# Performance work log

Measured on AMD Instinct MI355X. Metric: run time of the kernel, lower is better.

The kernel has to match this reference:

```python
import jax, jax.numpy as jnp
import numpy as np

DIM, H, DH, MLP, ADIM = 512, 8, 64, 2048, 256
B, T = 4, 2048
EPS = 1e-5


def setup_inputs() -> dict:
    key = jax.random.key(0)
    ks = jax.random.split(key, 10)
    s = 0.02
    inner = H * DH
    return {
        "x": jax.random.normal(ks[0], (B, T, DIM), jnp.float32),
        "action_emb": jax.random.normal(ks[1], (B, T, ADIM), jnp.float32),
        "causal_mask": jnp.tril(jnp.ones((T, T), dtype=bool)),
        "Wqkv": jax.random.normal(ks[2], (3 * inner, DIM), jnp.float32) * s,
        "Wout": jax.random.normal(ks[3], (DIM, inner), jnp.float32) * s,
        "bout": jnp.zeros((DIM,), jnp.float32),
        "W1": jax.random.normal(ks[4], (MLP, DIM), jnp.float32) * s,
        "b1": jnp.zeros((MLP,), jnp.float32),
        "W2": jax.random.normal(ks[5], (DIM, MLP), jnp.float32) * s,
        "b2": jnp.zeros((DIM,), jnp.float32),
        # adaLN is zero-init in the module; use small random so modulation is exercised
        "Wmod": jax.random.normal(ks[6], (6 * DIM, ADIM), jnp.float32) * s,
        "bmod": jnp.zeros((6 * DIM,), jnp.float32),
    }


def _layernorm(z):
    mu = jnp.mean(z, axis=-1, keepdims=True)
    var = jnp.var(z, axis=-1, keepdims=True)
    return (z - mu) * jax.lax.rsqrt(var + EPS)


def reference(x, action_emb, causal_mask, Wqkv, Wout, bout, W1, b1, W2, b2, Wmod, bmod):
    b, t, d = x.shape
    mod = jax.nn.silu(action_emb) @ Wmod.T + bmod            # (B,T,6*dim)
    shift1, scale1, gate1, shift2, scale2, gate2 = jnp.split(mod, 6, axis=-1)

    h = _layernorm(x) * (1.0 + scale1) + shift1
    qkv = (h @ Wqkv.T).reshape(b, t, 3, H, DH)
    q, k, v = qkv[:, :, 0], qkv[:, :, 1], qkv[:, :, 2]        # (B,T,H,DH)
    scores = jnp.einsum("bqhd,bkhd->bhqk", q, k) * (DH ** -0.5)
    scores = jnp.where(causal_mask, scores, -jnp.inf)
    attn = jax.nn.softmax(scores, axis=-1)                   # dropout=eval (identity)
    h = jnp.einsum("bhqk,bkhd->bqhd", attn, v).reshape(b, t, H * DH)
    h = h @ Wout.T + bout
    x = x + gate1 * h

    h = _layernorm(x) * (1.0 + scale2) + shift2
    h = jax.nn.gelu(h @ W1.T + b1, approximate=False) @ W2.T + b2
    return x + gate2 * h
```

## Files before the change

kernel.cpp:

```cpp
#include <hip/hip_runtime.h>
#include <math.h>
#include <stdint.h>

#define BB 4
#define TT 2048
#define NTOK 8192
#define DIMD 512
#define HH 8
#define DHH 64
#define MLPD 2048
#define ADIMD 256
#define MODD 3072
#define LNEPS 1e-5f
#define LOG2E_8 0.18033688011112042f

typedef short short8 __attribute__((ext_vector_type(8)));
typedef unsigned short ushort4v __attribute__((ext_vector_type(4)));
typedef __bf16 bf16x8 __attribute__((ext_vector_type(8)));
typedef float f32x4 __attribute__((ext_vector_type(4)));

static __device__ __forceinline__ unsigned short f2bf(float f) {
    union { float f; unsigned u; } v; v.f = f;
    unsigned r = v.u + 0x7fffu + ((v.u >> 16) & 1u);
    return (unsigned short)(r >> 16);
}
static __device__ __forceinline__ float bf2f(unsigned short u) {
    union { unsigned u; float f; } v; v.u = (unsigned)u << 16; return v.f;
}

static __device__ __forceinline__ f32x4 mfma_bf16(short8 a, short8 b, f32x4 c) {
    return __builtin_amdgcn_mfma_f32_16x16x32_bf16(
        __builtin_bit_cast(bf16x8, a), __builtin_bit_cast(bf16x8, b), c, 0, 0, 0);
}

struct CvtArgs {
    const float* s[6];
    unsigned short* d[6];
    int cum[7];
};
__global__ __launch_bounds__(256) void cvt_all(CvtArgs a)
{
    const int i = blockIdx.x * 256 + threadIdx.x;
    if (i >= a.cum[6]) return;
    int seg = 0;
    #pragma unroll
    for (int k = 1; k < 6; k++) seg += (i >= a.cum[k]);
    const int off = i - a.cum[seg];
    float4 v = ((const float4*)a.s[seg])[off];
    if (seg == 5) {
        v.x = v.x / (1.f + __expf(-v.x));
        v.y = v.y / (1.f + __expf(-v.y));
        v.z = v.z / (1.f + __expf(-v.z));
        v.w = v.w / (1.f + __expf(-v.w));
    }
    ushort4v o = { f2bf(v.x), f2bf(v.y), f2bf(v.z), f2bf(v.w) };
    ((ushort4v*)a.d[seg])[off] = o;
}

template<int EPI, int BN>
__global__ __launch_bounds__(256) void gemm_bf16(
    const unsigned short* __restrict__ A, const unsigned short* __restrict__ Bw,
    const float* __restrict__ bias, const float* __restrict__ res,
    const unsigned short* __restrict__ mod,
    int M, int N, int K,
    void* __restrict__ Cv)
{
    constexpr int MT = (BN == 128) ? 4 : 2;
    constexpr int NPB = (BN == 128) ? 4 : 2;
    __shared__ unsigned short As[128 * 72];
    __shared__ unsigned short Bs[BN * 72];

    const int tid = threadIdx.x;
    const int w = tid >> 6, lane = tid & 63;
    const int quad = lane >> 4, l16 = lane & 15;
    const int wrow = (BN == 128) ? (w >> 1) * 64 : w * 32;
    const int wcol = (BN == 128) ? (w & 1) * 64 : 0;
    const int row0 = blockIdx.y * 128, col0 = blockIdx.x * BN;

    const int srow = tid >> 3;
    const int skc  = (tid & 7) * 8;

    f32x4 acc[MT][4];
    #pragma unroll
    for (int i = 0; i < MT; i++)
        #pragma unroll
        for (int j = 0; j < 4; j++) acc[i][j] = (f32x4){0.f, 0.f, 0.f, 0.f};

    short8 pA[4], pB[NPB];
    auto prefetch = [&](int k0) {
        #pragma unroll
        for (int p = 0; p < 4; p++)
            pA[p] = *(const short8*)&A[(size_t)(row0 + srow + p * 32) * K + k0 + skc];
        #pragma unroll
        for (int p = 0; p < NPB; p++)
            pB[p] = *(const short8*)&Bw[(size_t)(col0 + srow + p * 32) * K + k0 + skc];
    };
    auto stage = [&]() {
        #pragma unroll
        for (int p = 0; p < 4; p++)
            *(short8*)&As[(srow + p * 32) * 72 + skc] = pA[p];
        #pragma unroll
        for (int p = 0; p < NPB; p++)
            *(short8*)&Bs[(srow + p * 32) * 72 + skc] = pB[p];
    };

    prefetch(0);
    stage();
    __syncthreads();

    for (int k0 = 0; k0 < K; k0 += 64) {
        const bool more = (k0 + 64 < K);
        if (more) prefetch(k0 + 64);

        #pragma unroll
        for (int ks = 0; ks < 2; ks++) {
            short8 af[MT], bf[4];
            #pragma unroll
            for (int mt = 0; mt < MT; mt++)
                af[mt] = *(const short8*)&As[(wrow + mt * 16 + l16) * 72 + ks * 32 + quad * 8];
            #pragma unroll
            for (int nt = 0; nt < 4; nt++)
                bf[nt] = *(const short8*)&Bs[(wcol + nt * 16 + l16) * 72 + ks * 32 + quad * 8];
            #pragma unroll
            for (int nt = 0; nt < 4; nt++)
                #pragma unroll
                for (int mt = 0; mt < MT; mt++)
                    acc[mt][nt] = mfma_bf16(af[mt], bf[nt], acc[mt][nt]);
        }
        __syncthreads();
        if (more) stage();
        __syncthreads();
    }

    float* Cf = (float*)Cv;
    unsigned short* Cb = (unsigned short*)Cv;
    #pragma unroll
    for (int mt = 0; mt < MT; mt++) {
        #pragma unroll
        for (int r = 0; r < 4; r++) {
            const int row = row0 + wrow + mt * 16 + quad * 4 + r;
            #pragma unroll
            for (int nt = 0; nt < 4; nt++) {
                const int col = col0 + wcol + nt * 16 + l16;
                const size_t idx = (size_t)row * N + col;
                const float v = acc[mt][nt][r];
                if (EPI == 0) {
                    Cb[idx] = f2bf(v);
                } else if (EPI == 2) {
                    float t = v + bias[col];
                    Cb[idx] = f2bf(0.5f * t * (1.f + erff(t * 0.70710678118654752f)));
                } else if (EPI == 3) {
                    float t = v + bias[col];
                    Cf[idx] = res[idx] + bf2f(mod[(size_t)row * MODD + 1024 + col]) * t;
                } else if (EPI == 4) {
                    float t = v + bias[col];
                    Cf[idx] = Cf[idx] + bf2f(mod[(size_t)row * MODD + 2560 + col]) * t;
                } else if (EPI == 5) {
                    Cb[idx] = f2bf(v + bias[col]);
                }
            }
        }
    }
}

__global__ __launch_bounds__(256) void adaln_ln(
    const float* __restrict__ src, const unsigned short* __restrict__ mod,
    unsigned short* __restrict__ dst, int shift_off, int scale_off)
{
    const int n = blockIdx.x;
    const int tid = threadIdx.x;
    const float* xr = src + (size_t)n * DIMD;
    float v0 = xr[tid], v1 = xr[tid + 256];
    float s = v0 + v1;
    float q = v0 * v0 + v1 * v1;
    #pragma unroll
    for (int o = 32; o > 0; o >>= 1) {
        s += __shfl_down(s, o);
        q += __shfl_down(q, o);
    }
    __shared__ float sh[8];
    __shared__ float mu_sh, rs_sh;
    const int wid = tid >> 6, lane = tid & 63;
    if (lane == 0) { sh[wid] = s; sh[wid + 4] = q; }
    __syncthreads();
    if (tid == 0) {
        float S = sh[0] + sh[1] + sh[2] + sh[3];
        float Q = sh[4] + sh[5] + sh[6] + sh[7];
        float mu = S * (1.f / DIMD);
        float var = Q * (1.f / DIMD) - mu * mu;
        mu_sh = mu;
        rs_sh = rsqrtf(var + LNEPS);
    }
    __syncthreads();
    const float mu = mu_sh, rs = rs_sh;
    const unsigned short* mrow = mod + (size_t)n * MODD;
    const size_t o0 = (size_t)n * DIMD + tid;
    dst[o0]       = f2bf((v0 - mu) * rs * (1.f + bf2f(mrow[scale_off + tid]))       + bf2f(mrow[shift_off + tid]));
    dst[o0 + 256] = f2bf((v1 - mu) * rs * (1.f + bf2f(mrow[scale_off + tid + 256])) + bf2f(mrow[shift_off + tid + 256]));
}

__global__ __launch_bounds__(256, 4) void attn_mfma(
    const unsigned short* __restrict__ qkv, unsigned short* __restrict__ outb)
{
    __shared__ unsigned short Kt[64][72];
    __shared__ unsigned short Vt[64][72];
    __shared__ unsigned short Ps[4][16][72];

    const int qi = (TT / 64 - 1) - blockIdx.x;
    const int h = blockIdx.y, b = blockIdx.z;
    const int tid = threadIdx.x;
    const int w = tid >> 6;
    const int lane = tid & 63;
    const int quad = lane >> 4;
    const int l16 = lane & 15;

    const int qw = qi * 64 + w * 16;
    const size_t tokbase = (size_t)b * TT;

    short8 qf[2];
    {
        const unsigned short* qp = qkv + (tokbase + qw + l16) * 1536 + h * 64 + quad * 8;
        #pragma unroll
        for (int hd = 0; hd < 2; hd++) {
            short8 raw = *(const short8*)(qp + hd * 32);
            short8 f;
            #pragma unroll
            for (int j = 0; j < 8; j++)
                f[j] = (short)f2bf(bf2f((unsigned short)raw[j]) * LOG2E_8);
            qf[hd] = f;
        }
    }

    f32x4 Oa[4];
    float mrun = -INFINITY, lrun = 0.f;
    #pragma unroll
    for (int mt = 0; mt < 4; mt++) Oa[mt] = (f32x4){0.f, 0.f, 0.f, 0.f};

    const int nkt = qi + 1;
    const int vk0 = (tid & 31) * 2;
    const int vdb = (tid >> 5) * 8;

    short8 kpre[2], vpre[2];
    auto prefetchKV = [&](int kt) {
        const unsigned short* kb = qkv + (tokbase + (size_t)kt * 64) * 1536 + 512 + h * 64;
        #pragma unroll
        for (int it = 0; it < 2; it++) {
            const int i = tid + it * 256;
            kpre[it] = *(const short8*)(kb + (size_t)(i >> 3) * 1536 + (i & 7) * 8);
        }
        const unsigned short* vb = qkv + (tokbase + (size_t)kt * 64 + vk0) * 1536 + 1024 + h * 64 + vdb;
        vpre[0] = *(const short8*)vb;
        vpre[1] = *(const short8*)(vb + 1536);
    };
    auto storeKV = [&]() {
        #pragma unroll
        for (int it = 0; it < 2; it++) {
            const int i = tid + it * 256;
            *(short8*)&Kt[i >> 3][(i & 7) * 8] = kpre[it];
        }
        #pragma unroll
        for (int j = 0; j < 8; j++) {
            *(unsigned*)&Vt[vdb + j][vk0] =
                (unsigned)(unsigned short)vpre[0][j]
                | ((unsigned)(unsigned short)vpre[1][j] << 16);
        }
    };

    prefetchKV(0);
    storeKV();
    __syncthreads();

    for (int kt = 0; kt < nkt; kt++) {
        const bool haveNext = (kt + 1 < nkt);
        if (haveNext) prefetchKV(kt + 1);

        f32x4 st[4];
        #pragma unroll
        for (int mk = 0; mk < 4; mk++) {
            const short8 a0 = *(const short8*)&Kt[mk * 16 + l16][quad * 8];
            const short8 a1 = *(const short8*)&Kt[mk * 16 + l16][32 + quad * 8];
            st[mk] = (f32x4){0.f, 0.f, 0.f, 0.f};
            st[mk] = mfma_bf16(a0, qf[0], st[mk]);
            st[mk] = mfma_bf16(a1, qf[1], st[mk]);
        }
        if (kt == qi) {
            const int qpos = qw + l16;
            #pragma unroll
            for (int mk = 0; mk < 4; mk++)
                #pragma unroll
                for (int r = 0; r < 4; r++)
                    if (kt * 64 + mk * 16 + quad * 4 + r > qpos) st[mk][r] = -INFINITY;
        }
        float tm = -INFINITY;
        #pragma unroll
        for (int mk = 0; mk < 4; mk++)
            #pragma unroll
            for (int r = 0; r < 4; r++) tm = fmaxf(tm, st[mk][r]);
        tm = fmaxf(tm, __shfl_xor(tm, 16));
        tm = fmaxf(tm, __shfl_xor(tm, 32));
        const float mn = fmaxf(mrun, tm);
        const float alpha = __builtin_amdgcn_exp2f(mrun - mn);
        mrun = mn;
        float ts = 0.f;
        #pragma unroll
        for (int mk = 0; mk < 4; mk++) {
            const float p0 = __builtin_amdgcn_exp2f(st[mk][0] - mn);
            const float p1 = __builtin_amdgcn_exp2f(st[mk][1] - mn);
            const float p2 = __builtin_amdgcn_exp2f(st[mk][2] - mn);
            const float p3 = __builtin_amdgcn_exp2f(st[mk][3] - mn);
            ts += (p0 + p1) + (p2 + p3);
            const unsigned long long pk =
                (unsigned long long)f2bf(p0)
                | ((unsigned long long)f2bf(p1) << 16)
                | ((unsigned long long)f2bf(p2) << 32)
                | ((unsigned long long)f2bf(p3) << 48);
            *(unsigned long long*)&Ps[w][l16][mk * 16 + quad * 4] = pk;
        }
        ts += __shfl_xor(ts, 16);
        ts += __shfl_xor(ts, 32);
        lrun = lrun * alpha + ts;
        #pragma unroll
        for (int mt = 0; mt < 4; mt++) Oa[mt] *= alpha;
        __threadfence_block();

        short8 pf[2];
        #pragma unroll
        for (int kc = 0; kc < 2; kc++)
            pf[kc] = *(const short8*)&Ps[w][l16][kc * 32 + quad * 8];
        #pragma unroll
        for (int mt = 0; mt < 4; mt++)
            #pragma unroll
            for (int kc = 0; kc < 2; kc++) {
                const short8 vf = *(const short8*)&Vt[mt * 16 + l16][kc * 32 + quad * 8];
                Oa[mt] = mfma_bf16(vf, pf[kc], Oa[mt]);
            }

        __syncthreads();
        if (haveNext) storeKV();
        __syncthreads();
    }

    {
        const float inv = 1.f / lrun;
        const size_t tok = tokbase + qw + l16;
        #pragma unroll
        for (int mt = 0; mt < 4; mt++) {
            const unsigned long long pk =
                (unsigned long long)f2bf(Oa[mt][0] * inv)
                | ((unsigned long long)f2bf(Oa[mt][1] * inv) << 16)
                | ((unsigned long long)f2bf(Oa[mt][2] * inv) << 32)
                | ((unsigned long long)f2bf(Oa[mt][3] * inv) << 48);
            *(unsigned long long*)&outb[tok * DIMD + h * 64 + mt * 16 + quad * 4] = pk;
        }
    }
}

extern "C" void kernel_launch(void* const* d_in, const int* in_sizes, int n_in,
                              void* d_out, int out_size, void* d_ws, size_t ws_size,
                              hipStream_t stream)
{
    (void)in_sizes; (void)n_in; (void)out_size; (void)ws_size;

    const float* x    = (const float*)d_in[0];
    const float* aemb = (const float*)d_in[1];
    const float* Wqkv = (const float*)d_in[3];
    const float* Wout = (const float*)d_in[4];
    const float* bout = (const float*)d_in[5];
    const float* W1   = (const float*)d_in[6];
    const float* b1   = (const float*)d_in[7];
    const float* W2   = (const float*)d_in[8];
    const float* b2   = (const float*)d_in[9];
    const float* Wmod = (const float*)d_in[10];
    const float* bmod = (const float*)d_in[11];

    float* out = (float*)d_out;

    char* p = (char*)d_ws;
    unsigned short* modw = (unsigned short*)p; p += (size_t)NTOK * MODD * 2;
    unsigned short* h12  = (unsigned short*)p; p += (size_t)NTOK * DIMD * 2;
    unsigned short* qkvb = (unsigned short*)p; p += (size_t)NTOK * 1536 * 2;
    unsigned short* attw = (unsigned short*)p; p += (size_t)NTOK * DIMD * 2;
    unsigned short* hid  = qkvb;
    unsigned short* sact = (unsigned short*)p; p += (size_t)NTOK * ADIMD * 2;
    unsigned short* wq = (unsigned short*)p;   p += (size_t)1536 * 512 * 2;
    unsigned short* wo = (unsigned short*)p;   p += (size_t)512 * 512 * 2;
    unsigned short* w1 = (unsigned short*)p;   p += (size_t)2048 * 512 * 2;
    unsigned short* w2 = (unsigned short*)p;   p += (size_t)512 * 2048 * 2;
    unsigned short* wm = (unsigned short*)p;   p += (size_t)3072 * 256 * 2;

    CvtArgs ca;
    ca.s[0] = Wqkv; ca.d[0] = wq;
    ca.s[1] = Wout; ca.d[1] = wo;
    ca.s[2] = W1;   ca.d[2] = w1;
    ca.s[3] = W2;   ca.d[3] = w2;
    ca.s[4] = Wmod; ca.d[4] = wm;
    ca.s[5] = aemb; ca.d[5] = sact;
    const int n4s[6] = {1536 * 512 / 4, 512 * 512 / 4, 2048 * 512 / 4,
                        512 * 2048 / 4, 3072 * 256 / 4, NTOK * ADIMD / 4};
    ca.cum[0] = 0;
    for (int i = 0; i < 6; i++) ca.cum[i + 1] = ca.cum[i] + n4s[i];
    cvt_all<<<(ca.cum[6] + 255) / 256, 256, 0, stream>>>(ca);

    gemm_bf16<5, 128><<<dim3(MODD / 128, NTOK / 128), 256, 0, stream>>>(
        sact, wm, bmod, nullptr, nullptr, NTOK, MODD, ADIMD, modw);

    adaln_ln<<<NTOK, 256, 0, stream>>>(x, modw, h12, 0, 512);

    gemm_bf16<0, 128><<<dim3(1536 / 128, NTOK / 128), 256, 0, stream>>>(
        h12, wq, nullptr, nullptr, nullptr, NTOK, 1536, DIMD, qkvb);

    attn_mfma<<<dim3(TT / 64, HH, BB), 256, 0, stream>>>(qkvb, attw);

    gemm_bf16<3, 64><<<dim3(DIMD / 64, NTOK / 128), 256, 0, stream>>>(
        attw, wo, bout, x, modw, NTOK, DIMD, DIMD, out);

    adaln_ln<<<NTOK, 256, 0, stream>>>(out, modw, h12, 1536, 2048);

    gemm_bf16<2, 128><<<dim3(MLPD / 128, NTOK / 128), 256, 0, stream>>>(
        h12, w1, b1, nullptr, nullptr, NTOK, MLPD, DIMD, hid);

    gemm_bf16<4, 64><<<dim3(DIMD / 64, NTOK / 128), 256, 0, stream>>>(
        hid, w2, b2, nullptr, modw, NTOK, DIMD, MLPD, out);
}
```

Before: 337.8 us.

## Deepen register prefetch to two tiles in GEMM and attention loops

Both the GEMM main loop and the flash-attention KV loop now keep two register-staged tiles in flight, so global loads run two iterations ahead instead of one. __syncthreads is replaced with a barrier that only waits on LDS counters, which lets outstanding global loads stay in flight across barriers. The goal is to hide more global-memory latency. The cost is roughly double the prefetch registers, which may lower occupancy, and the GEMM loop assumes an even K-tile count.

```diff
diff --git a/kernel.cpp b/kernel.cpp
--- a/kernel.cpp
+++ b/kernel.cpp
@@ -31,6 +31,10 @@
 static __device__ __forceinline__ f32x4 mfma_bf16(short8 a, short8 b, f32x4 c) {
     return __builtin_amdgcn_mfma_f32_16x16x32_bf16(
         __builtin_bit_cast(bf16x8, a), __builtin_bit_cast(bf16x8, b), c, 0, 0, 0);
+}
+
+static __device__ __forceinline__ void bar_lds() {
+    asm volatile("s_waitcnt lgkmcnt(0)\n\ts_barrier" ::: "memory");
 }
 
 struct CvtArgs {
@@ -86,51 +90,58 @@
         #pragma unroll
         for (int j = 0; j < 4; j++) acc[i][j] = (f32x4){0.f, 0.f, 0.f, 0.f};
 
-    short8 pA[4], pB[NPB];
-    auto prefetch = [&](int k0) {
-        #pragma unroll
-        for (int p = 0; p < 4; p++)
-            pA[p] = *(const short8*)&A[(size_t)(row0 + srow + p * 32) * K + k0 + skc];
-        #pragma unroll
-        for (int p = 0; p < NPB; p++)
-            pB[p] = *(const short8*)&Bw[(size_t)(col0 + srow + p * 32) * K + k0 + skc];
-    };
-    auto stage = [&]() {
-        #pragma unroll
-        for (int p = 0; p < 4; p++)
-            *(short8*)&As[(srow + p * 32) * 72 + skc] = pA[p];
-        #pragma unroll
-        for (int p = 0; p < NPB; p++)
-            *(short8*)&Bs[(srow + p * 32) * 72 + skc] = pB[p];
-    };
-
-    prefetch(0);
-    stage();
-    __syncthreads();
-
-    for (int k0 = 0; k0 < K; k0 += 64) {
-        const bool more = (k0 + 64 < K);
-        if (more) prefetch(k0 + 64);
-
-        #pragma unroll
-        for (int ks = 0; ks < 2; ks++) {
-            short8 af[MT], bf[4];
-            #pragma unroll
-            for (int mt = 0; mt < MT; mt++)
-                af[mt] = *(const short8*)&As[(wrow + mt * 16 + l16) * 72 + ks * 32 + quad * 8];
-            #pragma unroll
-            for (int nt = 0; nt < 4; nt++)
-                bf[nt] = *(const short8*)&Bs[(wcol + nt * 16 + l16) * 72 + ks * 32 + quad * 8];
-            #pragma unroll
-            for (int nt = 0; nt < 4; nt++)
-                #pragma unroll
-                for (int mt = 0; mt < MT; mt++)
-                    acc[mt][nt] = mfma_bf16(af[mt], bf[nt], acc[mt][nt]);
+    short8 a0[4], b0[NPB], a1[4], b1[NPB];
+
+#define G_LOAD(AS_, BS_, k0_) do {                                              \
+    _Pragma("unroll") for (int p = 0; p < 4; p++)                               \
+        AS_[p] = *(const short8*)&A[(size_t)(row0 + srow + p * 32) * K + (k0_) + skc]; \
+    _Pragma("unroll") for (int p = 0; p < NPB; p++)                             \
+        BS_[p] = *(const short8*)&Bw[(size_t)(col0 + srow + p * 32) * K + (k0_) + skc]; \
+} while (0)
+
+#define G_STAGE(AS_, BS_) do {                                                  \
+    _Pragma("unroll") for (int p = 0; p < 4; p++)                               \
+        *(short8*)&As[(srow + p * 32) * 72 + skc] = AS_[p];                     \
+    _Pragma("unroll") for (int p = 0; p < NPB; p++)                             \
+        *(short8*)&Bs[(srow + p * 32) * 72 + skc] = BS_[p];                     \
+} while (0)
+
+#define G_COMPUTE() do {                                                        \
+    _Pragma("unroll") for (int ks = 0; ks < 2; ks++) {                          \
+        short8 af[MT], bf[4];                                                   \
+        _Pragma("unroll") for (int mt = 0; mt < MT; mt++)                       \
+            af[mt] = *(const short8*)&As[(wrow + mt * 16 + l16) * 72 + ks * 32 + quad * 8]; \
+        _Pragma("unroll") for (int nt = 0; nt < 4; nt++)                        \
+            bf[nt] = *(const short8*)&Bs[(wcol + nt * 16 + l16) * 72 + ks * 32 + quad * 8]; \
+        _Pragma("unroll") for (int nt = 0; nt < 4; nt++)                        \
+            _Pragma("unroll") for (int mt = 0; mt < MT; mt++)                   \
+                acc[mt][nt] = mfma_bf16(af[mt], bf[nt], acc[mt][nt]);           \
+    }                                                                           \
+} while (0)
+
+    const int NK = K >> 6;
+    G_LOAD(a0, b0, 0);
+    G_LOAD(a1, b1, 64);
+    G_STAGE(a0, b0);
+    bar_lds();
+
+    for (int t = 0; t < NK; t += 2) {
+        if (t + 2 < NK) G_LOAD(a0, b0, (t + 2) << 6);
+        G_COMPUTE();
+        bar_lds();
+        G_STAGE(a1, b1);
+        bar_lds();
+        if (t + 3 < NK) G_LOAD(a1, b1, (t + 3) << 6);
+        G_COMPUTE();
+        if (t + 2 < NK) {
+            bar_lds();
+            G_STAGE(a0, b0);
+            bar_lds();
         }
-        __syncthreads();
-        if (more) stage();
-        __syncthreads();
-    }
+    }
+#undef G_LOAD
+#undef G_STAGE
+#undef G_COMPUTE
 
     float* Cf = (float*)Cv;
     unsigned short* Cb = (unsigned short*)Cv;
@@ -240,105 +251,105 @@
     const int vk0 = (tid & 31) * 2;
     const int vdb = (tid >> 5) * 8;
 
-    short8 kpre[2], vpre[2];
-    auto prefetchKV = [&](int kt) {
-        const unsigned short* kb = qkv + (tokbase + (size_t)kt * 64) * 1536 + 512 + h * 64;
-        #pragma unroll
-        for (int it = 0; it < 2; it++) {
-            const int i = tid + it * 256;
-            kpre[it] = *(const short8*)(kb + (size_t)(i >> 3) * 1536 + (i & 7) * 8);
-        }
-        const unsigned short* vb = qkv + (tokbase + (size_t)kt * 64 + vk0) * 1536 + 1024 + h * 64 + vdb;
-        vpre[0] = *(const short8*)vb;
-        vpre[1] = *(const short8*)(vb + 1536);
-    };
-    auto storeKV = [&]() {
-        #pragma unroll
-        for (int it = 0; it < 2; it++) {
-            const int i = tid + it * 256;
-            *(short8*)&Kt[i >> 3][(i & 7) * 8] = kpre[it];
-        }
-        #pragma unroll
-        for (int j = 0; j < 8; j++) {
-            *(unsigned*)&Vt[vdb + j][vk0] =
-                (unsigned)(unsigned short)vpre[0][j]
-                | ((unsigned)(unsigned short)vpre[1][j] << 16);
-        }
-    };
-
-    prefetchKV(0);
-    storeKV();
-    __syncthreads();
-
-    for (int kt = 0; kt < nkt; kt++) {
-        const bool haveNext = (kt + 1 < nkt);
-        if (haveNext) prefetchKV(kt + 1);
-
-        f32x4 st[4];
-        #pragma unroll
-        for (int mk = 0; mk < 4; mk++) {
-            const short8 a0 = *(const short8*)&Kt[mk * 16 + l16][quad * 8];
-            const short8 a1 = *(const short8*)&Kt[mk * 16 + l16][32 + quad * 8];
-            st[mk] = (f32x4){0.f, 0.f, 0.f, 0.f};
-            st[mk] = mfma_bf16(a0, qf[0], st[mk]);
-            st[mk] = mfma_bf16(a1, qf[1], st[mk]);
-        }
-        if (kt == qi) {
-            const int qpos = qw + l16;
-            #pragma unroll
-            for (int mk = 0; mk < 4; mk++)
-                #pragma unroll
-                for (int r = 0; r < 4; r++)
-                    if (kt * 64 + mk * 16 + quad * 4 + r > qpos) st[mk][r] = -INFINITY;
-        }
-        float tm = -INFINITY;
-        #pragma unroll
-        for (int mk = 0; mk < 4; mk++)
-            #pragma unroll
-            for (int r = 0; r < 4; r++) tm = fmaxf(tm, st[mk][r]);
-        tm = fmaxf(tm, __shfl_xor(tm, 16));
-        tm = fmaxf(tm, __shfl_xor(tm, 32));
-        const float mn = fmaxf(mrun, tm);
-        const float alpha = __builtin_amdgcn_exp2f(mrun - mn);
-        mrun = mn;
-        float ts = 0.f;
-        #pragma unroll
-        for (int mk = 0; mk < 4; mk++) {
-            const float p0 = __builtin_amdgcn_exp2f(st[mk][0] - mn);
-            const float p1 = __builtin_amdgcn_exp2f(st[mk][1] - mn);
-            const float p2 = __builtin_amdgcn_exp2f(st[mk][2] - mn);
-            const float p3 = __builtin_amdgcn_exp2f(st[mk][3] - mn);
-            ts += (p0 + p1) + (p2 + p3);
-            const unsigned long long pk =
-                (unsigned long long)f2bf(p0)
-                | ((unsigned long long)f2bf(p1) << 16)
-                | ((unsigned long long)f2bf(p2) << 32)
-                | ((unsigned long long)f2bf(p3) << 48);
-            *(unsigned long long*)&Ps[w][l16][mk * 16 + quad * 4] = pk;
-        }
-        ts += __shfl_xor(ts, 16);
-        ts += __shfl_xor(ts, 32);
-        lrun = lrun * alpha + ts;
-        #pragma unroll
-        for (int mt = 0; mt < 4; mt++) Oa[mt] *= alpha;
-        __threadfence_block();
-
-        short8 pf[2];
-        #pragma unroll
-        for (int kc = 0; kc < 2; kc++)
-            pf[kc] = *(const short8*)&Ps[w][l16][kc * 32 + quad * 8];
-        #pragma unroll
-        for (int mt = 0; mt < 4; mt++)
-            #pragma unroll
-            for (int kc = 0; kc < 2; kc++) {
-                const short8 vf = *(const short8*)&Vt[mt * 16 + l16][kc * 32 + quad * 8];
-                Oa[mt] = mfma_bf16(vf, pf[kc], Oa[mt]);
-            }
-
-        __syncthreads();
-        if (haveNext) storeKV();
-        __syncthreads();
-    }
+    short8 kp0[2], vp0[2], kp1[2], vp1[2];
+
+#define A_LOAD(KS_, VS_, kt_) do {                                              \
+    const unsigned short* kb = qkv + (tokbase + (size_t)(kt_) * 64) * 1536 + 512 + h * 64; \
+    _Pragma("unroll") for (int it = 0; it < 2; it++) {                          \
+        const int i = tid + it * 256;                                           \
+        KS_[it] = *(const short8*)(kb + (size_t)(i >> 3) * 1536 + (i & 7) * 8); \
+    }                                                                           \
+    const unsigned short* vb = qkv + (tokbase + (size_t)(kt_) * 64 + vk0) * 1536 + 1024 + h * 64 + vdb; \
+    VS_[0] = *(const short8*)vb;                                                \
+    VS_[1] = *(const short8*)(vb + 1536);                                       \
+} while (0)
+
+#define A_STAGE(KS_, VS_) do {                                                  \
+    _Pragma("unroll") for (int it = 0; it < 2; it++) {                          \
+        const int i = tid + it * 256;                                           \
+        *(short8*)&Kt[i >> 3][(i & 7) * 8] = KS_[it];                           \
+    }                                                                           \
+    _Pragma("unroll") for (int j = 0; j < 8; j++) {                             \
+        *(unsigned*)&Vt[vdb + j][vk0] =                                         \
+            (unsigned)(unsigned short)VS_[0][j]                                 \
+            | ((unsigned)(unsigned short)VS_[1][j] << 16);                      \
+    }                                                                           \
+} while (0)
+
+#define A_COMPUTE(kt_) do {                                                     \
+    f32x4 st[4];                                                                \
+    _Pragma("unroll") for (int mk = 0; mk < 4; mk++) {                          \
+        const short8 ka0 = *(const short8*)&Kt[mk * 16 + l16][quad * 8];        \
+        const short8 ka1 = *(const short8*)&Kt[mk * 16 + l16][32 + quad * 8];   \
+        st[mk] = (f32x4){0.f, 0.f, 0.f, 0.f};                                   \
+        st[mk] = mfma_bf16(ka0, qf[0], st[mk]);                                 \
+        st[mk] = mfma_bf16(ka1, qf[1], st[mk]);                                 \
+    }                                                                           \
+    if ((kt_) == qi) {                                                          \
+        const int qpos = qw + l16;                                              \
+        _Pragma("unroll") for (int mk = 0; mk < 4; mk++)                        \
+            _Pragma("unroll") for (int r = 0; r < 4; r++)                       \
+                if ((kt_) * 64 + mk * 16 + quad * 4 + r > qpos) st[mk][r] = -INFINITY; \
+    }                                                                           \
+    float tm = -INFINITY;                                                       \
+    _Pragma("unroll") for (int mk = 0; mk < 4; mk++)                            \
+        _Pragma("unroll") for (int r = 0; r < 4; r++) tm = fmaxf(tm, st[mk][r]);\
+    tm = fmaxf(tm, __shfl_xor(tm, 16));                                         \
+    tm = fmaxf(tm, __shfl_xor(tm, 32));                                         \
+    const float mn = fmaxf(mrun, tm);                                           \
+    const float alpha = __builtin_amdgcn_exp2f(mrun - mn);                      \
+    mrun = mn;                                                                  \
+    float ts = 0.f;                                                             \
+    _Pragma("unroll") for (int mk = 0; mk < 4; mk++) {                          \
+        const float p0 = __builtin_amdgcn_exp2f(st[mk][0] - mn);                \
+        const float p1 = __builtin_amdgcn_exp2f(st[mk][1] - mn);                \
+        const float p2 = __builtin_amdgcn_exp2f(st[mk][2] - mn);                \
+        const float p3 = __builtin_amdgcn_exp2f(st[mk][3] - mn);                \
+        ts += (p0 + p1) + (p2 + p3);                                            \
+        const unsigned long long pk =                                           \
+            (unsigned long long)f2bf(p0)                                        \
+            | ((unsigned long long)f2bf(p1) << 16)                              \
+            | ((unsigned long long)f2bf(p2) << 32)                              \
+            | ((unsigned long long)f2bf(p3) << 48);                             \
+        *(unsigned long long*)&Ps[w][l16][mk * 16 + quad * 4] = pk;             \
+    }                                                                           \
+    ts += __shfl_xor(ts, 16);                                                   \
+    ts += __shfl_xor(ts, 32);                                                   \
+    lrun = lrun * alpha + ts;                                                   \
+    _Pragma("unroll") for (int mt = 0; mt < 4; mt++) Oa[mt] *= alpha;           \
+    __threadfence_block();                                                      \
+    short8 pf[2];                                                               \
+    _Pragma("unroll") for (int kc = 0; kc < 2; kc++)                            \
+        pf[kc] = *(const short8*)&Ps[w][l16][kc * 32 + quad * 8];               \
+    _Pragma("unroll") for (int mt = 0; mt < 4; mt++)                            \
+        _Pragma("unroll") for (int kc = 0; kc < 2; kc++) {                      \
+            const short8 vf = *(const short8*)&Vt[mt * 16 + l16][kc * 32 + quad * 8]; \
+            Oa[mt] = mfma_bf16(vf, pf[kc], Oa[mt]);                             \
+        }                                                                       \
+} while (0)
+
+    A_LOAD(kp0, vp0, 0);
+    if (nkt > 1) A_LOAD(kp1, vp1, 1);
+    A_STAGE(kp0, vp0);
+    bar_lds();
+
+    int t = 0;
+    while (t < nkt) {
+        if (t + 2 < nkt) A_LOAD(kp0, vp0, t + 2);
+        A_COMPUTE(t);
+        bar_lds();
+        if (t + 1 < nkt) { A_STAGE(kp1, vp1); bar_lds(); }
+        t++;
+        if (t >= nkt) break;
+        if (t + 2 < nkt) A_LOAD(kp1, vp1, t + 2);
+        A_COMPUTE(t);
+        bar_lds();
+        if (t + 1 < nkt) { A_STAGE(kp0, vp0); bar_lds(); }
+        t++;
+    }
+#undef A_LOAD
+#undef A_STAGE
+#undef A_COMPUTE
 
     {
         const float inv = 1.f / lrun;
```

Result: slower. 383.7 us (+13.6%).
